# Kernel tuning notes

Measured on AMD Instinct MI355X. Metric: run time of the kernel, lower is better.

The kernel has to match this reference:

```python
import jax, jax.numpy as jnp
import numpy as np

B, T, D, U = 64, 512, 512, 512  # units must equal input feature dim (concat along axis -2)


def setup_inputs() -> dict:
    key = jax.random.key(0)
    ks = jax.random.split(key, 5)
    glorot = float(np.sqrt(2.0 / (D + U)))  # glorot_normal std
    x = jax.random.normal(ks[0], (B, T, D), dtype=jnp.float32)
    Wq = jax.random.normal(ks[1], (D, U), dtype=jnp.float32) * glorot
    Wk = jax.random.normal(ks[2], (D, U), dtype=jnp.float32) * glorot
    Wv = jax.random.normal(ks[3], (D, U), dtype=jnp.float32) * glorot
    Wrec = jax.random.normal(ks[4], (U, U), dtype=jnp.float32) * glorot
    return {"x": x, "Wq": Wq, "Wk": Wk, "Wv": Wv, "Wrec": Wrec}


def reference(x, Wq, Wk, Wv, Wrec):
    # Self_RNN forward (inference: dropout mask == ones).
    # Recurrent step over time:
    #   hist = h @ Wrec ; inp3 = stack([hist, prev_input, x_t]) -> (B,3,D)
    #   Q,K,V = inp3 @ {Wq,Wk,Wv}                              -> (B,3,U)
    #   keras batch_dot(key^T, query, axes=[1,2]) => scores[b,i,j] = K[b,i]·Q[b,j]
    #   softmax over j (the query axis); output row i=0 only:
    #   out = sum_j softmax_j(K[b,0]·Q[b,j]/sqrt(U)) * V[b,j]
    #   new states: (out, x_t).  K.rnn -> return last output.
    units = Wq.shape[1]
    scale = 1.0 / jnp.sqrt(jnp.asarray(units, x.dtype))

    def step(carry, x_t):
        h, prev = carry
        hist = h @ Wrec                               # (B,U)
        inp3 = jnp.stack([hist, prev, x_t], axis=1)   # (B,3,D)
        Q = inp3 @ Wq                                 # (B,3,U)
        K0 = inp3[:, 0] @ Wk                          # only key row 0 (hist) is used
        V = inp3 @ Wv                                 # (B,3,U)
        scores = jnp.einsum('bu,bju->bj', K0, Q) * scale   # (B,3)
        attn = jax.nn.softmax(scores, axis=-1)
        out = jnp.einsum('bj,bju->bu', attn, V)       # (B,U)
        return (out, x_t), None

    h0 = jnp.zeros((x.shape[0], units), x.dtype)
    p0 = jnp.zeros((x.shape[0], x.shape[-1]), x.dtype)
    (h_last, _), _ = jax.lax.scan(step, (h0, p0), jnp.swapaxes(x, 0, 1))
    return h_last
```

## Files before the change

### kernel.cpp

```cpp
#include <hip/hip_runtime.h>


typedef _Float16 f16;
typedef _Float16 half8 __attribute__((ext_vector_type(8)));
typedef _Float16 h2 __attribute__((ext_vector_type(2)));
typedef float floatx4 __attribute__((ext_vector_type(4)));
typedef unsigned long long u64;

#define AM_F32 0
#define AM_F16 1
#define BM_NN_F32 0
#define BM_BT_F16 1
#define BM_BT_F32 2

#if defined(__has_builtin)
#if __has_builtin(__builtin_amdgcn_fdot2)
#define HAS_FDOT2 1
#endif
#endif

__device__ inline float dot2f(h2 a, h2 b, float c) {
#ifdef HAS_FDOT2
  return __builtin_amdgcn_fdot2(a, b, c, false);
#else
  return c + (float)a[0] * (float)b[0] + (float)a[1] * (float)b[1];
#endif
}

template<int AMODE, int BMODE, int CT>
__global__ __launch_bounds__(256)
void gemm128(const void* __restrict__ Ap, const void* __restrict__ Bp,
             f16* __restrict__ C, int K, int ldbnn, long ldc, long coff,
             int ntiles) {
  __shared__ f16 Al[128 * 32];
  __shared__ f16 Bl[128 * 32];
  const int tid = threadIdx.x;
  const int lane = tid & 63;
  const int wid = tid >> 6;
  const int wr = wid >> 1, wc = wid & 1;
  const int mt = blockIdx.x / ntiles, nt = blockIdx.x % ntiles;
  const long m0 = (long)mt * 128, n0 = (long)nt * 128;

  floatx4 acc[4][4];
#pragma unroll
  for (int m = 0; m < 4; ++m)
#pragma unroll
    for (int n = 0; n < 4; ++n) acc[m][n] = (floatx4){0.f, 0.f, 0.f, 0.f};

  for (int k0 = 0; k0 < K; k0 += 32) {
    __syncthreads();
#pragma unroll
    for (int i = 0; i < 2; ++i) {
      const int slot = i * 256 + tid;
      const int row = slot >> 2;
      const int kc = (slot & 3) * 8;
      if constexpr (AMODE == AM_F16) {
        const f16* Ag = (const f16*)Ap;
        half8 v = *(const half8*)(Ag + (m0 + row) * (long)K + k0 + kc);
        *(half8*)(Al + slot * 8) = v;
      } else {
        const float* Ag = (const float*)Ap;
        const float* p = Ag + (m0 + row) * (long)K + k0 + kc;
        float4 v0 = *(const float4*)(p);
        float4 v1 = *(const float4*)(p + 4);
        half8 h;
        h[0] = (f16)v0.x; h[1] = (f16)v0.y; h[2] = (f16)v0.z; h[3] = (f16)v0.w;
        h[4] = (f16)v1.x; h[5] = (f16)v1.y; h[6] = (f16)v1.z; h[7] = (f16)v1.w;
        *(half8*)(Al + slot * 8) = h;
      }
    }
    if constexpr (BMODE == BM_NN_F32) {
      const float* Bg = (const float*)Bp;
      const int nn = tid & 127;
      const int kh = (tid >> 7) * 16;
#pragma unroll
      for (int j = 0; j < 16; j += 2) {
        float b0 = Bg[(long)(k0 + kh + j) * ldbnn + n0 + nn];
        float b1 = Bg[(long)(k0 + kh + j + 1) * ldbnn + n0 + nn];
        h2 hv; hv[0] = (f16)b0; hv[1] = (f16)b1;
        *(h2*)(Bl + nn * 32 + kh + j) = hv;
      }
    } else {
#pragma unroll
      for (int i = 0; i < 2; ++i) {
        const int slot = i * 256 + tid;
        const int row = slot >> 2;
        const int kc = (slot & 3) * 8;
        if constexpr (BMODE == BM_BT_F16) {
          const f16* Bg = (const f16*)Bp;
          half8 v = *(const half8*)(Bg + (n0 + row) * (long)K + k0 + kc);
          *(half8*)(Bl + slot * 8) = v;
        } else {
          const float* Bg = (const float*)Bp;
          const float* p = Bg + (n0 + row) * (long)K + k0 + kc;
          float4 v0 = *(const float4*)(p);
          float4 v1 = *(const float4*)(p + 4);
          half8 h;
          h[0] = (f16)v0.x; h[1] = (f16)v0.y; h[2] = (f16)v0.z; h[3] = (f16)v0.w;
          h[4] = (f16)v1.x; h[5] = (f16)v1.y; h[6] = (f16)v1.z; h[7] = (f16)v1.w;
          *(half8*)(Bl + slot * 8) = h;
        }
      }
    }
    __syncthreads();
    const int frow = lane & 15;
    const int fkc = (lane >> 4) * 8;
    half8 af[4], bf[4];
#pragma unroll
    for (int m = 0; m < 4; ++m)
      af[m] = *(const half8*)(Al + (wr * 64 + m * 16 + frow) * 32 + fkc);
#pragma unroll
    for (int n = 0; n < 4; ++n)
      bf[n] = *(const half8*)(Bl + (wc * 64 + n * 16 + frow) * 32 + fkc);
#pragma unroll
    for (int m = 0; m < 4; ++m)
#pragma unroll
      for (int n = 0; n < 4; ++n)
        acc[m][n] = __builtin_amdgcn_mfma_f32_16x16x32_f16(af[m], bf[n],
                                                           acc[m][n], 0, 0, 0);
  }
  const int crow = (lane >> 4) * 4;
  const int ccol = lane & 15;
#pragma unroll
  for (int m = 0; m < 4; ++m)
#pragma unroll
    for (int n = 0; n < 4; ++n)
#pragma unroll
      for (int r = 0; r < 4; ++r) {
        long row = m0 + wr * 64 + m * 16 + crow + r;
        long col = n0 + wc * 64 + n * 16 + ccol;
        if constexpr (CT)
          C[(coff + col) * ldc + row] = (f16)acc[m][n][r];
        else
          C[row * ldc + coff + col] = (f16)acc[m][n][r];
      }
}

__global__ void zero_ybuf(u64* ybuf) {
  ybuf[(size_t)blockIdx.x * 256 + threadIdx.x] = 0ull;
}

__global__ __launch_bounds__(256, 1)
void seq_kernel(const f16* __restrict__ Wt, const f16* __restrict__ GXV,
                u64* __restrict__ ybuf, float* __restrict__ out) {
  const int wg = blockIdx.x;
  const int grp = wg & 15;
  const int s = wg >> 4;
  const int tid = threadIdx.x;
  const int lane = tid & 63;
  const int wid = tid >> 6;
  const int T = 512;

  __shared__ __align__(16) char wlds[64 * 1024];
  __shared__ __align__(16) char hpkb[16 * 1024];
  __shared__ float yredf[4 * 256];
  __shared__ float swred[4][8];
  __shared__ float aa[4][4];

  {
    const int col = tid >> 2;
    const int seg = (tid & 3) * 256;
    const unsigned key = ((unsigned)col & 7u) << 4;
    const char* src = (const char*)(Wt + (size_t)(s * 64 + col) * 512);
#pragma unroll
    for (int k = 0; k < 16; ++k) {
      half8 v = *(const half8*)(src + seg + k * 16);
      *(half8*)(wlds + col * 1024 + ((unsigned)(seg + k * 16) ^ key)) = v;
    }
  }
#pragma unroll
  for (int i = 0; i < 4; ++i)
    *(floatx4*)(hpkb + tid * 64 + i * 16) = (floatx4){0.f, 0.f, 0.f, 0.f};
  __syncthreads();

  const float scale = 0.04419417382415922f;
  const bool isV = (s < 8);
  u64* const yVp = ybuf;
  u64* const s0p = ybuf + 32768;

  const int arow = lane & 15;
  const unsigned abkey = ((unsigned)(arow & 7)) << 4;
  const int kbase = wid * 256 + (lane >> 4) * 16;

  for (int t = 0; t < T; ++t) {
    const int par = t & 1;
    const u64 tagw = ((u64)(unsigned)(t + 1)) << 32;

    h2 xc4[4], xp4[4], gcv[4], gpv[4];
#pragma unroll
    for (int c4 = 0; c4 < 4; ++c4) {
      const f16* rowc = GXV + (((size_t)grp * 4 + c4) * T + t) * 1024;
      gcv[c4] = *(const h2*)(rowc + 2 * tid);
      xc4[c4] = *(const h2*)(rowc + 512 + 2 * tid);
      h2 z; z[0] = (f16)0.f; z[1] = (f16)0.f;
      gpv[c4] = z; xp4[c4] = z;
      if (t > 0) {
        gpv[c4] = *(const h2*)(rowc - 1024 + 2 * tid);
        xp4[c4] = *(const h2*)(rowc - 512 + 2 * tid);
      }
    }

    {
      floatx4 acc[4];
#pragma unroll
      for (int nt = 0; nt < 4; ++nt) acc[nt] = (floatx4){0.f, 0.f, 0.f, 0.f};
#pragma unroll
      for (int i = 0; i < 4; ++i) {
        const unsigned ko = (unsigned)(kbase + i * 64);
        half8 av = *(const half8*)(hpkb + arow * 1024 + (ko ^ abkey));
#pragma unroll
        for (int nt = 0; nt < 4; ++nt) {
          half8 bv = *(const half8*)(wlds + (nt * 16 + arow) * 1024 + (ko ^ abkey));
          acc[nt] = __builtin_amdgcn_mfma_f32_16x16x32_f16(av, bv, acc[nt], 0, 0, 0);
        }
      }
      if (lane < 16) {
#pragma unroll
        for (int nt = 0; nt < 4; ++nt)
          *(floatx4*)&yredf[wid * 256 + (nt * 16 + lane) * 4] = acc[nt];
      }
    }

    {
      float pr[8];
#pragma unroll
      for (int c4 = 0; c4 < 4; ++c4) {
        h2 hv = *(const h2*)(hpkb + c4 * 1024 +
                             (((unsigned)(4 * tid)) ^ (((unsigned)c4) << 4)));
        pr[2 * c4] = dot2f(gpv[c4], hv, 0.f);
        pr[2 * c4 + 1] = dot2f(gcv[c4], hv, 0.f);
      }
#pragma unroll
      for (int off = 32; off > 0; off >>= 1)
#pragma unroll
        for (int i = 0; i < 8; ++i) pr[i] += __shfl_down(pr[i], off);
      if (lane == 0) {
#pragma unroll
        for (int i = 0; i < 8; ++i) swred[wid][i] = pr[i];
      }
    }
    __syncthreads();

    if (isV) {
      float y = yredf[tid] + yredf[256 + tid] + yredf[512 + tid] + yredf[768 + tid];
      float yp = __shfl_down(y, 4);
      if ((tid & 4) == 0) {
        h2 pk; pk[0] = (f16)y; pk[1] = (f16)yp;
        unsigned lo; __builtin_memcpy(&lo, &pk, 4);
        __hip_atomic_store(
            yVp + (((size_t)grp * 2 + par) * 4 + (tid & 3)) * 256 + s * 32 + (tid >> 3),
            tagw | (u64)lo, __ATOMIC_RELAXED, __HIP_MEMORY_SCOPE_AGENT);
      }
    } else {
      const int lc = lane;
      float yq = yredf[lc * 4 + wid] + yredf[256 + lc * 4 + wid] +
                 yredf[512 + lc * 4 + wid] + yredf[768 + lc * 4 + wid];
      const int u = (s - 8) * 64 + lc;
      f16 hu = *(const f16*)(hpkb + wid * 1024 +
                             (((unsigned)(2 * u)) ^ (((unsigned)wid) << 4)));
      float p = yq * (float)hu;
#pragma unroll
      for (int off = 32; off > 0; off >>= 1) p += __shfl_down(p, off);
      if (lane == 0)
        __hip_atomic_store(
            s0p + (((size_t)grp * 2 + par) * 4 + wid) * 8 + (s - 8),
            tagw | (u64)__float_as_uint(p), __ATOMIC_RELAXED,
            __HIP_MEMORY_SCOPE_AGENT);
    }

    const u64* vb = yVp + (((size_t)grp * 2 + par) * 4) * 256 + tid;
    u64 v0, v1, v2, v3, sw = tagw;
    const u64* sb = s0p + (((size_t)grp * 2 + par) * 4 + (tid >> 3)) * 8 + (tid & 7);
    for (;;) {
      v0 = __hip_atomic_load(vb, __ATOMIC_RELAXED, __HIP_MEMORY_SCOPE_AGENT);
      v1 = __hip_atomic_load(vb + 256, __ATOMIC_RELAXED, __HIP_MEMORY_SCOPE_AGENT);
      v2 = __hip_atomic_load(vb + 512, __ATOMIC_RELAXED, __HIP_MEMORY_SCOPE_AGENT);
      v3 = __hip_atomic_load(vb + 768, __ATOMIC_RELAXED, __HIP_MEMORY_SCOPE_AGENT);
      bool ok = (v0 >= tagw) & (v1 >= tagw) & (v2 >= tagw) & (v3 >= tagw);
      if (tid < 32) {
        sw = __hip_atomic_load(sb, __ATOMIC_RELAXED, __HIP_MEMORY_SCOPE_AGENT);
        ok = ok && (sw >= tagw);
      }
      if (ok) break;
      __builtin_amdgcn_s_sleep(1);
    }

    if (tid < 32) {
      float sp = __uint_as_float((unsigned)sw);
      sp += __shfl_xor(sp, 1);
      sp += __shfl_xor(sp, 2);
      sp += __shfl_xor(sp, 4);
      if ((tid & 7) == 0) {
        const int c4 = tid >> 3;
        const float sv0 = sp * scale;
        const float sv1 = (swred[0][2 * c4] + swred[1][2 * c4] +
                           swred[2][2 * c4] + swred[3][2 * c4]) * scale;
        const float sv2 = (swred[0][2 * c4 + 1] + swred[1][2 * c4 + 1] +
                           swred[2][2 * c4 + 1] + swred[3][2 * c4 + 1]) * scale;
        const float mx = fmaxf(sv0, fmaxf(sv1, sv2));
        const float e0 = __expf(sv0 - mx), e1 = __expf(sv1 - mx),
                    e2 = __expf(sv2 - mx);
        const float inv = 1.f / (e0 + e1 + e2);
        aa[c4][0] = e0 * inv; aa[c4][1] = e1 * inv; aa[c4][2] = e2 * inv;
      }
    }
    __syncthreads();

    {
      u64 vw[4] = {v0, v1, v2, v3};
#pragma unroll
      for (int c4 = 0; c4 < 4; ++c4) {
        const float a0 = aa[c4][0], a1 = aa[c4][1], a2 = aa[c4][2];
        unsigned lo = (unsigned)vw[c4];
        h2 vh; __builtin_memcpy(&vh, &lo, 4);
        float hn0 = a0 * (float)vh[0] + a1 * (float)xp4[c4][0] + a2 * (float)xc4[c4][0];
        float hn1 = a0 * (float)vh[1] + a1 * (float)xp4[c4][1] + a2 * (float)xc4[c4][1];
        h2 hn; hn[0] = (f16)hn0; hn[1] = (f16)hn1;
        *(h2*)(hpkb + c4 * 1024 +
               (((unsigned)(4 * tid)) ^ (((unsigned)c4) << 4))) = hn;
        if (t == T - 1 && s == 0) {
          float* ob = out + ((size_t)grp * 4 + c4) * 512 + 2 * tid;
          ob[0] = hn0; ob[1] = hn1;
        }
      }
    }
    __syncthreads();
  }
}

extern "C" void kernel_launch(void* const* d_in, const int* in_sizes, int n_in,
                              void* d_out, int out_size, void* d_ws,
                              size_t ws_size, hipStream_t stream) {
  const float* x = (const float*)d_in[0];
  const float* Wq = (const float*)d_in[1];
  const float* Wk = (const float*)d_in[2];
  const float* Wv = (const float*)d_in[3];
  const float* Wrec = (const float*)d_in[4];
  float* out = (float*)d_out;

  char* ws = (char*)d_ws;
  f16* GXV = (f16*)ws;
  f16* Wt = (f16*)(ws + 67108864);
  f16* Wrk = (f16*)(ws + 68157440);
  f16* Wrq = (f16*)(ws + 68681728);
  f16* WgT = (f16*)(ws + 69206016);
  u64* ybuf = (u64*)(ws + 68681728);

  gemm128<AM_F32, BM_NN_F32, 0><<<16, 256, 0, stream>>>(Wrec, Wk, Wrk, 512, 512, 512, 0, 4);
  gemm128<AM_F32, BM_NN_F32, 0><<<16, 256, 0, stream>>>(Wrec, Wq, Wrq, 512, 512, 512, 0, 4);
  gemm128<AM_F32, BM_NN_F32, 1><<<16, 256, 0, stream>>>(Wrec, Wv, Wt, 512, 512, 512, 0, 4);
  gemm128<AM_F16, BM_BT_F16, 1><<<16, 256, 0, stream>>>(Wrk, Wrq, Wt, 512, 0, 512, 512, 4);
  gemm128<AM_F16, BM_BT_F32, 0><<<16, 256, 0, stream>>>(Wrk, Wq, WgT, 512, 0, 512, 0, 4);
  gemm128<AM_F32, BM_BT_F16, 0><<<1024, 256, 0, stream>>>(x, WgT, GXV, 512, 0, 1024, 0, 4);
  gemm128<AM_F32, BM_NN_F32, 0><<<1024, 256, 0, stream>>>(x, Wv, GXV, 512, 512, 1024, 512, 4);

  zero_ybuf<<<132, 256, 0, stream>>>(ybuf);

  const f16* WtC = Wt; const f16* GXVC = GXV;
  void* args[] = {(void*)&WtC, (void*)&GXVC, (void*)&ybuf, (void*)&out};
  dim3 grid(256), block(256);
  if (hipLaunchCooperativeKernel((const void*)seq_kernel, grid, block, args, 0,
                                 stream) != hipSuccess) {
    seq_kernel<<<grid, block, 0, stream>>>(WtC, GXVC, ybuf, out);
  }
}
```

Baseline: 1.957 ms.

## Split recurrent matvec by output columns per wave, drop LDS cross-wave reduction

Each wave now computes the full K=512 reduction for its own 16 output columns instead of splitting K across waves and reducing partial sums through shared memory. Results are published straight from registers to the global exchange buffer, and the score path writes per-wave partials that the consumer sums with extra shuffle stages. This removes the yredf shared array, its reduction, and the barrier before publishing. In exchange each wave runs a longer serial chain of MFMAs, the consumer polls more flags, and the zeroed buffer region grows.

```diff
diff --git a/kernel.cpp b/kernel.cpp
--- a/kernel.cpp
+++ b/kernel.cpp
@@ -153,7 +153,6 @@
 
   __shared__ __align__(16) char wlds[64 * 1024];
   __shared__ __align__(16) char hpkb[16 * 1024];
-  __shared__ float yredf[4 * 256];
   __shared__ float swred[4][8];
   __shared__ float aa[4][4];
 
@@ -180,7 +179,7 @@
 
   const int arow = lane & 15;
   const unsigned abkey = ((unsigned)(arow & 7)) << 4;
-  const int kbase = wid * 256 + (lane >> 4) * 16;
+  const int kseg = (lane >> 4) * 16;
 
   for (int t = 0; t < T; ++t) {
     const int par = t & 1;
@@ -200,24 +199,49 @@
       }
     }
 
-    {
-      floatx4 acc[4];
-#pragma unroll
-      for (int nt = 0; nt < 4; ++nt) acc[nt] = (floatx4){0.f, 0.f, 0.f, 0.f};
-#pragma unroll
-      for (int i = 0; i < 4; ++i) {
-        const unsigned ko = (unsigned)(kbase + i * 64);
-        half8 av = *(const half8*)(hpkb + arow * 1024 + (ko ^ abkey));
-#pragma unroll
-        for (int nt = 0; nt < 4; ++nt) {
-          half8 bv = *(const half8*)(wlds + (nt * 16 + arow) * 1024 + (ko ^ abkey));
-          acc[nt] = __builtin_amdgcn_mfma_f32_16x16x32_f16(av, bv, acc[nt], 0, 0, 0);
+    floatx4 acc = (floatx4){0.f, 0.f, 0.f, 0.f};
+#pragma unroll
+    for (int ks = 0; ks < 16; ++ks) {
+      const unsigned ko = (unsigned)(ks * 64 + kseg);
+      half8 av = *(const half8*)(hpkb + arow * 1024 + (ko ^ abkey));
+      half8 bv = *(const half8*)(wlds + (wid * 16 + arow) * 1024 + (ko ^ abkey));
+      acc = __builtin_amdgcn_mfma_f32_16x16x32_f16(av, bv, acc, 0, 0, 0);
+    }
+
+    if (isV) {
+#pragma unroll
+      for (int r = 0; r < 4; ++r) {
+        float v = acc[r];
+        float vp = __shfl_xor(v, 1);
+        if (lane < 16 && !(lane & 1)) {
+          h2 pk; pk[0] = (f16)v; pk[1] = (f16)vp;
+          unsigned lo; __builtin_memcpy(&lo, &pk, 4);
+          __hip_atomic_store(
+              yVp + (((size_t)grp * 2 + par) * 4 + r) * 256 + s * 32 + wid * 8 +
+                  (lane >> 1),
+              tagw | (u64)lo, __ATOMIC_RELAXED, __HIP_MEMORY_SCOPE_AGENT);
         }
       }
-      if (lane < 16) {
-#pragma unroll
-        for (int nt = 0; nt < 4; ++nt)
-          *(floatx4*)&yredf[wid * 256 + (nt * 16 + lane) * 4] = acc[nt];
+    } else {
+      float p[4];
+      const int c = (s - 8) * 64 + wid * 16 + arow;
+#pragma unroll
+      for (int r = 0; r < 4; ++r) {
+        f16 hv = *(const f16*)(hpkb + r * 1024 +
+                               (((unsigned)(2 * c)) ^ (((unsigned)r) << 4)));
+        p[r] = acc[r] * (float)hv;
+      }
+#pragma unroll
+      for (int off = 32; off > 0; off >>= 1)
+#pragma unroll
+        for (int r = 0; r < 4; ++r) p[r] += __shfl_down(p[r], off);
+      if (lane == 0) {
+#pragma unroll
+        for (int r = 0; r < 4; ++r)
+          __hip_atomic_store(
+              s0p + (((size_t)grp * 2 + par) * 4 + r) * 32 + (s - 8) * 4 + wid,
+              tagw | (u64)__float_as_uint(p[r]), __ATOMIC_RELAXED,
+              __HIP_MEMORY_SCOPE_AGENT);
       }
     }
 
@@ -241,43 +265,16 @@
     }
     __syncthreads();
 
-    if (isV) {
-      float y = yredf[tid] + yredf[256 + tid] + yredf[512 + tid] + yredf[768 + tid];
-      float yp = __shfl_down(y, 4);
-      if ((tid & 4) == 0) {
-        h2 pk; pk[0] = (f16)y; pk[1] = (f16)yp;
-        unsigned lo; __builtin_memcpy(&lo, &pk, 4);
-        __hip_atomic_store(
-            yVp + (((size_t)grp * 2 + par) * 4 + (tid & 3)) * 256 + s * 32 + (tid >> 3),
-            tagw | (u64)lo, __ATOMIC_RELAXED, __HIP_MEMORY_SCOPE_AGENT);
-      }
-    } else {
-      const int lc = lane;
-      float yq = yredf[lc * 4 + wid] + yredf[256 + lc * 4 + wid] +
-                 yredf[512 + lc * 4 + wid] + yredf[768 + lc * 4 + wid];
-      const int u = (s - 8) * 64 + lc;
-      f16 hu = *(const f16*)(hpkb + wid * 1024 +
-                             (((unsigned)(2 * u)) ^ (((unsigned)wid) << 4)));
-      float p = yq * (float)hu;
-#pragma unroll
-      for (int off = 32; off > 0; off >>= 1) p += __shfl_down(p, off);
-      if (lane == 0)
-        __hip_atomic_store(
-            s0p + (((size_t)grp * 2 + par) * 4 + wid) * 8 + (s - 8),
-            tagw | (u64)__float_as_uint(p), __ATOMIC_RELAXED,
-            __HIP_MEMORY_SCOPE_AGENT);
-    }
-
     const u64* vb = yVp + (((size_t)grp * 2 + par) * 4) * 256 + tid;
+    const u64* sb = s0p + (((size_t)grp * 2 + par) * 4 + (tid >> 5)) * 32 + (tid & 31);
     u64 v0, v1, v2, v3, sw = tagw;
-    const u64* sb = s0p + (((size_t)grp * 2 + par) * 4 + (tid >> 3)) * 8 + (tid & 7);
     for (;;) {
       v0 = __hip_atomic_load(vb, __ATOMIC_RELAXED, __HIP_MEMORY_SCOPE_AGENT);
       v1 = __hip_atomic_load(vb + 256, __ATOMIC_RELAXED, __HIP_MEMORY_SCOPE_AGENT);
       v2 = __hip_atomic_load(vb + 512, __ATOMIC_RELAXED, __HIP_MEMORY_SCOPE_AGENT);
       v3 = __hip_atomic_load(vb + 768, __ATOMIC_RELAXED, __HIP_MEMORY_SCOPE_AGENT);
       bool ok = (v0 >= tagw) & (v1 >= tagw) & (v2 >= tagw) & (v3 >= tagw);
-      if (tid < 32) {
+      if (tid < 128) {
         sw = __hip_atomic_load(sb, __ATOMIC_RELAXED, __HIP_MEMORY_SCOPE_AGENT);
         ok = ok && (sw >= tagw);
       }
@@ -285,13 +282,15 @@
       __builtin_amdgcn_s_sleep(1);
     }
 
-    if (tid < 32) {
+    if (tid < 128) {
       float sp = __uint_as_float((unsigned)sw);
       sp += __shfl_xor(sp, 1);
       sp += __shfl_xor(sp, 2);
       sp += __shfl_xor(sp, 4);
-      if ((tid & 7) == 0) {
-        const int c4 = tid >> 3;
+      sp += __shfl_xor(sp, 8);
+      sp += __shfl_xor(sp, 16);
+      if ((tid & 31) == 0) {
+        const int c4 = tid >> 5;
         const float sv0 = sp * scale;
         const float sv1 = (swred[0][2 * c4] + swred[1][2 * c4] +
                            swred[2][2 * c4] + swred[3][2 * c4]) * scale;
@@ -354,7 +353,7 @@
   gemm128<AM_F32, BM_BT_F16, 0><<<1024, 256, 0, stream>>>(x, WgT, GXV, 512, 0, 1024, 0, 4);
   gemm128<AM_F32, BM_NN_F32, 0><<<1024, 256, 0, stream>>>(x, Wv, GXV, 512, 512, 1024, 512, 4);
 
-  zero_ybuf<<<132, 256, 0, stream>>>(ybuf);
+  zero_ybuf<<<144, 256, 0, stream>>>(ybuf);
 
   const f16* WtC = Wt; const f16* GXVC = GXV;
   void* args[] = {(void*)&WtC, (void*)&GXVC, (void*)&ybuf, (void*)&out};
```

Measured after the change: 1.659 ms. 1.18x faster.
